# Performance work log

Measured on AMD Instinct MI355X. Metric: run time of the kernel, lower is better.

## Reference

```python
import jax, jax.numpy as jnp
import numpy as np

N_HEADS = 32
N_KV_HEADS = 8
HEAD_DIM = 64
D_MODEL = 2048
EPS = 1e-6
THETA = 10000.0


def _rms_norm(x, w):
    # normalize over last dim (head_dim)
    norm = jax.lax.rsqrt(jnp.mean(jnp.square(x), axis=-1, keepdims=True) + EPS)
    return x * norm * w


def _rope(x):
    # x: (B, H, T, D)
    T, D = x.shape[2], x.shape[3]
    inv_freq = 1.0 / (THETA ** (jnp.arange(0, D, 2, dtype=jnp.float32) / D))
    t = jnp.arange(T, dtype=jnp.float32)
    freqs = jnp.outer(t, inv_freq)                      # (T, D/2)
    freqs = jnp.concatenate([freqs, freqs], axis=-1)    # (T, D)
    cos = jnp.cos(freqs)[None, None]                    # (1,1,T,D)
    sin = jnp.sin(freqs)[None, None]
    x1, x2 = x[..., : D // 2], x[..., D // 2 :]
    x_rot = jnp.concatenate([-x2, x1], axis=-1)
    return x * cos + x_rot * sin


def setup_inputs() -> dict:
    key = jax.random.key(0)
    ks = jax.random.split(key, 5)
    B, T = 2, 2048
    s = 0.02
    return {
        "x": jax.random.normal(ks[0], (B, T, D_MODEL), jnp.float32),
        "wq": jax.random.normal(ks[1], (D_MODEL, D_MODEL), jnp.float32) * s,
        "wk": jax.random.normal(ks[2], (N_KV_HEADS * HEAD_DIM, D_MODEL), jnp.float32) * s,
        "wv": jax.random.normal(ks[3], (N_KV_HEADS * HEAD_DIM, D_MODEL), jnp.float32) * s,
        "wo": jax.random.normal(ks[4], (D_MODEL, D_MODEL), jnp.float32) * s,
        "q_norm_w": jnp.ones((HEAD_DIM,), jnp.float32),
        "k_norm_w": jnp.ones((HEAD_DIM,), jnp.float32),
    }


def reference(x, wq, wk, wv, wo, q_norm_w, k_norm_w):
    B, T, C = x.shape
    G = N_HEADS // N_KV_HEADS

    q = (x @ wq.T).reshape(B, T, N_HEADS, HEAD_DIM).transpose(0, 2, 1, 3)      # (B,H,T,D)
    k = (x @ wk.T).reshape(B, T, N_KV_HEADS, HEAD_DIM).transpose(0, 2, 1, 3)   # (B,KH,T,D)
    v = (x @ wv.T).reshape(B, T, N_KV_HEADS, HEAD_DIM).transpose(0, 2, 1, 3)

    q = _rms_norm(q, q_norm_w)
    k = _rms_norm(k, k_norm_w)

    q = _rope(q)
    k = _rope(k)

    # GQA head-expand: each kv head repeated G times consecutively
    k = jnp.repeat(k, G, axis=1)   # (B,H,T,D)
    v = jnp.repeat(v, G, axis=1)

    scale = 1.0 / np.sqrt(HEAD_DIM)
    scores = jnp.einsum("bhqd,bhkd->bhqk", q, k) * scale
    causal = jnp.tril(jnp.ones((T, T), dtype=bool))
    scores = jnp.where(causal[None, None], scores, jnp.finfo(scores.dtype).min)
    attn = jax.nn.softmax(scores, axis=-1)
    out = jnp.einsum("bhqk,bhkd->bhqd", attn, v)   # (B,H,T,D)

    out = out.transpose(0, 2, 1, 3).reshape(B, T, C)
    return out @ wo.T
```

## Files before the change

kernel.cpp:

```cpp
#include <hip/hip_runtime.h>

typedef __bf16 bf16;
typedef __bf16 bf16x8 __attribute__((ext_vector_type(8)));
typedef float f32x4 __attribute__((ext_vector_type(4)));

#define DEV __device__ __forceinline__

DEV void gload16(const void* g, void* l) {
  __builtin_amdgcn_global_load_lds(
      (__attribute__((address_space(1))) void*)g,
      (__attribute__((address_space(3))) void*)l,
      16, 0, 0);
}

DEV unsigned pack_bf16(float a, float b) {
  union { bf16 h[2]; unsigned u; } u;
  u.h[0] = (bf16)a; u.h[1] = (bf16)b;
  return u.u;
}

__global__ __launch_bounds__(256) void cvt_f32_to_bf16(
    const float* __restrict__ in, bf16* __restrict__ out, long n) {
  long i = ((long)blockIdx.x * 256 + threadIdx.x) * 8;
  if (i + 8 > n) return;
  const float4* p = (const float4*)(in + i);
  float4 a = p[0], b = p[1];
  bf16x8 o;
  o[0] = (bf16)a.x; o[1] = (bf16)a.y; o[2] = (bf16)a.z; o[3] = (bf16)a.w;
  o[4] = (bf16)b.x; o[5] = (bf16)b.y; o[6] = (bf16)b.z; o[7] = (bf16)b.w;
  *(bf16x8*)(out + i) = o;
}

template <typename OutT>
__global__ __launch_bounds__(512, 2) void gemm8p(
    const bf16* __restrict__ A, const bf16* __restrict__ B, OutT* __restrict__ C,
    int M, int N, int K) {
  __shared__ bf16 As[2][256 * 64];
  __shared__ bf16 Bs[2][256 * 64];
  const int tid = threadIdx.x;
  const int lane = tid & 63;
  const int wv = tid >> 6;
  const int wm = wv >> 2, wn = wv & 3;
  const int l15 = lane & 15, l4 = lane >> 4;
  const int swz7 = l15 & 7;
  const long m0 = (long)blockIdx.y * 256;
  const long n0 = (long)blockIdx.x * 256;
  const int NT = K >> 6;

  f32x4 acc[8][4];
#pragma unroll
  for (int i = 0; i < 8; ++i)
#pragma unroll
    for (int j = 0; j < 4; ++j) acc[i][j] = (f32x4){0.f, 0.f, 0.f, 0.f};

  auto stageA = [&](int t, int q) {
#pragma unroll
    for (int it = 0; it < 2; ++it) {
      const int c = it * 512 + tid;
      const int row = ((c >> 9) << 7) + q * 64 + ((c >> 3) & 63);
      const int cc = c & 7;
      gload16(A + (m0 + row) * (long)K + t * 64 + ((cc ^ (row & 7)) << 3),
              &As[t & 1][row * 64 + cc * 8]);
    }
  };
  auto stageB = [&](int t, int q) {
#pragma unroll
    for (int it = 0; it < 2; ++it) {
      const int c = it * 512 + tid;
      const int row = ((c >> 8) << 6) + q * 32 + ((c >> 3) & 31);
      const int cc = c & 7;
      gload16(B + (n0 + row) * (long)K + t * 64 + ((cc ^ (row & 7)) << 3),
              &Bs[t & 1][row * 64 + cc * 8]);
    }
  };

#define PHASE(CUR, QM, QN, STAGE, VM) do {                                      \
    __builtin_amdgcn_sched_barrier(0);                                          \
    bf16x8 af_[2][4], bf_[2][2];                                                \
    _Pragma("unroll")                                                           \
    for (int kk = 0; kk < 2; ++kk) {                                            \
      _Pragma("unroll")                                                         \
      for (int i = 0; i < 4; ++i)                                               \
        af_[kk][i] = *(const bf16x8*)&As[CUR][                                  \
            (wm * 128 + (QM) * 64 + i * 16 + l15) * 64 +                        \
            (((kk * 4 + l4) ^ swz7) << 3)];                                     \
      _Pragma("unroll")                                                         \
      for (int j = 0; j < 2; ++j)                                               \
        bf_[kk][j] = *(const bf16x8*)&Bs[CUR][                                  \
            (wn * 64 + (QN) * 32 + j * 16 + l15) * 64 +                         \
            (((kk * 4 + l4) ^ swz7) << 3)];                                     \
    }                                                                           \
    STAGE;                                                                      \
    VM;                                                                         \
    __builtin_amdgcn_sched_barrier(0);                                          \
    __builtin_amdgcn_s_barrier();                                               \
    asm volatile("s_waitcnt lgkmcnt(0)" ::: "memory");                          \
    __builtin_amdgcn_sched_barrier(0);                                          \
    __builtin_amdgcn_s_setprio(1);                                              \
    _Pragma("unroll")                                                           \
    for (int kk = 0; kk < 2; ++kk)                                              \
      _Pragma("unroll")                                                         \
      for (int i = 0; i < 4; ++i)                                               \
        _Pragma("unroll")                                                       \
        for (int j = 0; j < 2; ++j)                                             \
          acc[(QM) * 4 + i][(QN) * 2 + j] =                                     \
              __builtin_amdgcn_mfma_f32_16x16x32_bf16(                          \
                  af_[kk][i], bf_[kk][j], acc[(QM) * 4 + i][(QN) * 2 + j],      \
                  0, 0, 0);                                                     \
    __builtin_amdgcn_s_setprio(0);                                              \
    __builtin_amdgcn_s_barrier();                                               \
  } while (0)

  stageA(0, 0); stageA(0, 1); stageB(0, 0); stageB(0, 1);
  stageA(1, 0); stageB(1, 0);
  asm volatile("s_waitcnt vmcnt(4)" ::: "memory");
  __builtin_amdgcn_sched_barrier(0);
  __builtin_amdgcn_s_barrier();

  for (int T = 0; T < NT - 2; ++T) {
    const int cur = T & 1;
    PHASE(cur, 0, 0, stageA(T + 1, 1), );
    PHASE(cur, 0, 1, stageB(T + 1, 1), );
    PHASE(cur, 1, 0, stageA(T + 2, 0), );
    PHASE(cur, 1, 1, stageB(T + 2, 0),
          asm volatile("s_waitcnt vmcnt(4)" ::: "memory"));
  }
  {
    const int cur = (NT - 2) & 1;
    PHASE(cur, 0, 0, stageA(NT - 1, 1), );
    PHASE(cur, 0, 1, stageB(NT - 1, 1), );
    PHASE(cur, 1, 0, , );
    PHASE(cur, 1, 1, , asm volatile("s_waitcnt vmcnt(0)" ::: "memory"));
  }
  {
    const int cur = (NT - 1) & 1;
    PHASE(cur, 0, 0, , );
    PHASE(cur, 0, 1, , );
    PHASE(cur, 1, 0, , );
    PHASE(cur, 1, 1, , );
  }
#undef PHASE

#pragma unroll
  for (int i = 0; i < 8; ++i)
#pragma unroll
    for (int j = 0; j < 4; ++j) {
      const long row = m0 + wm * 128 + i * 16 + l4 * 4;
      const long col = n0 + wn * 64 + j * 16 + l15;
#pragma unroll
      for (int r = 0; r < 4; ++r)
        C[(row + r) * (long)N + col] = (OutT)acc[i][j][r];
    }
}

__global__ __launch_bounds__(256) void qk_norm_rope(
    const bf16* __restrict__ qkv, const float* __restrict__ qw,
    const float* __restrict__ kw, bf16* __restrict__ Qh, bf16* __restrict__ Kh) {
  const int wg = blockIdx.x * 4 + (threadIdx.x >> 6);
  const int lane = threadIdx.x & 63;
  const int row = wg / 40;
  const int head = wg - row * 40;
  const int b = row >> 11, t = row & 2047;
  const bool is_q = head < 32;
  const int col0 = is_q ? head * 64 : 2048 + (head - 32) * 64;

  float v = (float)qkv[(long)row * 3072 + col0 + lane];
  float ss = v * v;
  ss += __shfl_xor(ss, 1);
  ss += __shfl_xor(ss, 2);
  ss += __shfl_xor(ss, 4);
  ss += __shfl_xor(ss, 8);
  ss += __shfl_xor(ss, 16);
  ss += __shfl_xor(ss, 32);
  const float norm = rsqrtf(ss * (1.0f / 64.0f) + 1e-6f);
  const float* wn = is_q ? qw : kw;
  float xn = v * norm * wn[lane];

  const int fi = lane & 31;
  const float inv_freq = expf(-(float)fi * (9.210340371976184f / 32.0f));
  const float fr = (float)t * inv_freq;
  float sn, cs;
  sincosf(fr, &sn, &cs);
  const float xo = __shfl_xor(xn, 32);
  const float xr = (lane < 32) ? -xo : xo;
  const float res = xn * cs + xr * sn;

  if (is_q)
    Qh[(((long)b * 32 + head) * 2048 + t) * 64 + lane] = (bf16)res;
  else
    Kh[(((long)b * 8 + (head - 32)) * 2048 + t) * 64 + lane] = (bf16)res;
}

__global__ __launch_bounds__(256) void v_transpose(
    const bf16* __restrict__ qkv, bf16* __restrict__ Vt) {
  const int bh = blockIdx.x;
  const int t0 = blockIdx.y * 64;
  const int b = bh >> 3, kh = bh & 7;
  __shared__ bf16 tile[64][72];
  const int tid = threadIdx.x;
#pragma unroll
  for (int it = 0; it < 2; ++it) {
    const int tt = it * 32 + (tid >> 3);
    const int d0 = (tid & 7) * 8;
    bf16x8 val = *(const bf16x8*)&qkv[((long)b * 2048 + t0 + tt) * 3072 + 2560 + kh * 64 + d0];
#pragma unroll
    for (int j = 0; j < 8; ++j) tile[tt][d0 + j] = val[j];
  }
  __syncthreads();
#pragma unroll
  for (int it = 0; it < 2; ++it) {
    const int d = it * 32 + (tid >> 3);
    const int tb = (tid & 7) * 8;
    bf16x8 o;
#pragma unroll
    for (int j = 0; j < 8; ++j) o[j] = tile[tb + j][d];
    *(bf16x8*)&Vt[((long)bh * 64 + d) * 2048 + t0 + tb] = o;
  }
}

__global__ __launch_bounds__(256, 4) void attn_fwd(
    const bf16* __restrict__ Q, const bf16* __restrict__ K,
    const bf16* __restrict__ Vt, bf16* __restrict__ O) {
  const int b = blockIdx.x >> 5, h = blockIdx.x & 31;
  const int qb = 31 - (int)blockIdx.y;
  const int q0 = qb * 64;
  const int kvh = h >> 2;
  const bf16* Qp = Q + (((long)b * 32 + h) * 2048 + q0) * 64;
  const bf16* Kp = K + ((long)b * 8 + kvh) * (2048L * 64);
  const bf16* Vp = Vt + ((long)b * 8 + kvh) * (64L * 2048);

  __shared__ bf16 Ks[64 * 64];
  __shared__ bf16 Vs[64 * 64];

  const int tid = threadIdx.x, lane = tid & 63, w = tid >> 6;
  const int l15 = lane & 15, l4 = lane >> 4;
  const int qwr = q0 + w * 16;
  const int q_g = qwr + l15;

  bf16x8 qf[2];
#pragma unroll
  for (int kk = 0; kk < 2; ++kk)
    qf[kk] = *(const bf16x8*)(Qp + (w * 16 + l15) * 64 + kk * 32 + l4 * 8);

  f32x4 accO[4];
#pragma unroll
  for (int dn = 0; dn < 4; ++dn) accO[dn] = (f32x4){0.f, 0.f, 0.f, 0.f};
  float M = -1e30f, L = 0.f;

  const float scale = 0.125f;
  const int swz = (l15 & 7) << 3;

  for (int kt = 0; kt <= qb; ++kt) {
    const int k0 = kt * 64;
#pragma unroll
    for (int it = 0; it < 2; ++it) {
      const int c = it * 256 + tid;
      const int row = c >> 3, cc = c & 7;
      const int scol = ((cc ^ (row & 7)) << 3);
      gload16(Kp + (long)(k0 + row) * 64 + scol, &Ks[c * 8]);
      gload16(Vp + (long)row * 2048 + k0 + scol, &Vs[c * 8]);
    }
    __syncthreads();

    f32x4 sT[4];
#pragma unroll
    for (int n = 0; n < 4; ++n) sT[n] = (f32x4){0.f, 0.f, 0.f, 0.f};
#pragma unroll
    for (int kk = 0; kk < 2; ++kk) {
      bf16x8 kf[4];
#pragma unroll
      for (int n = 0; n < 4; ++n)
        kf[n] = *(const bf16x8*)&Ks[(n * 16 + l15) * 64 + (((kk * 4 + l4) << 3) ^ swz)];
#pragma unroll
      for (int n = 0; n < 4; ++n)
        sT[n] = __builtin_amdgcn_mfma_f32_16x16x32_bf16(kf[n], qf[kk], sT[n], 0, 0, 0);
    }

    const bool edge = (kt == qb);
#pragma unroll
    for (int n = 0; n < 4; ++n) {
      const int kbase = k0 + n * 16 + l4 * 4;
#pragma unroll
      for (int r = 0; r < 4; ++r) {
        float v = sT[n][r] * scale;
        if (edge && (kbase + r > q_g)) v = -1e30f;
        sT[n][r] = v;
      }
    }

    float pm = -1e30f;
#pragma unroll
    for (int n = 0; n < 4; ++n)
#pragma unroll
      for (int r = 0; r < 4; ++r) pm = fmaxf(pm, sT[n][r]);
    pm = fmaxf(pm, __shfl_xor(pm, 16));
    pm = fmaxf(pm, __shfl_xor(pm, 32));
    const float newM = fmaxf(M, pm);
    const float sc = __expf(M - newM);
    M = newM;
    float rs = 0.f;
#pragma unroll
    for (int n = 0; n < 4; ++n)
#pragma unroll
      for (int r = 0; r < 4; ++r) {
        const float pv = __expf(sT[n][r] - newM);
        sT[n][r] = pv;
        rs += pv;
      }
    rs += __shfl_xor(rs, 16);
    rs += __shfl_xor(rs, 32);
    L = L * sc + rs;
#pragma unroll
    for (int dn = 0; dn < 4; ++dn) accO[dn] *= sc;

    unsigned lo[4], hi[4];
#pragma unroll
    for (int n = 0; n < 4; ++n) {
      lo[n] = pack_bf16(sT[n][0], sT[n][1]);
      hi[n] = pack_bf16(sT[n][2], sT[n][3]);
    }

    const int srcA = l15 | ((l4 & 1) << 5);
    const int srcB = srcA + 16;
    const bool selHi = (l4 >> 1);
#pragma unroll
    for (int kk = 0; kk < 2; ++kk) {
      unsigned d0a = __shfl(lo[2 * kk], srcA), d0b = __shfl(lo[2 * kk + 1], srcA);
      unsigned d1a = __shfl(hi[2 * kk], srcA), d1b = __shfl(hi[2 * kk + 1], srcA);
      unsigned d2a = __shfl(lo[2 * kk], srcB), d2b = __shfl(lo[2 * kk + 1], srcB);
      unsigned d3a = __shfl(hi[2 * kk], srcB), d3b = __shfl(hi[2 * kk + 1], srcB);
      union { unsigned d[4]; bf16x8 v; } pu;
      pu.d[0] = selHi ? d0b : d0a;
      pu.d[1] = selHi ? d1b : d1a;
      pu.d[2] = selHi ? d2b : d2a;
      pu.d[3] = selHi ? d3b : d3a;
      bf16x8 vf[4];
#pragma unroll
      for (int dn = 0; dn < 4; ++dn)
        vf[dn] = *(const bf16x8*)&Vs[(dn * 16 + l15) * 64 + (((kk * 4 + l4) << 3) ^ swz)];
#pragma unroll
      for (int dn = 0; dn < 4; ++dn)
        accO[dn] = __builtin_amdgcn_mfma_f32_16x16x32_bf16(vf[dn], pu.v, accO[dn], 0, 0, 0);
    }
    __syncthreads();
  }

  const float inv = 1.0f / L;
  const long rowbase = ((long)b * 2048 + q_g) * 2048 + h * 64;
#pragma unroll
  for (int dn = 0; dn < 4; ++dn)
#pragma unroll
    for (int rp = 0; rp < 2; ++rp) {
      const unsigned pk = pack_bf16(accO[dn][2 * rp] * inv, accO[dn][2 * rp + 1] * inv);
      *(unsigned*)&O[rowbase + dn * 16 + l4 * 4 + 2 * rp] = pk;
    }
}

extern "C" void kernel_launch(void* const* d_in, const int* in_sizes, int n_in,
                              void* d_out, int out_size, void* d_ws, size_t ws_size,
                              hipStream_t stream) {
  const float* x   = (const float*)d_in[0];
  const float* wq  = (const float*)d_in[1];
  const float* wk  = (const float*)d_in[2];
  const float* wv  = (const float*)d_in[3];
  const float* wo  = (const float*)d_in[4];
  const float* qnw = (const float*)d_in[5];
  const float* knw = (const float*)d_in[6];
  float* out = (float*)d_out;

  char* ws = (char*)d_ws;
  size_t off = 0;
  auto carve = [&](size_t bytes) -> void* {
    void* p = ws + off;
    off += (bytes + 255) & ~(size_t)255;
    return p;
  };
  bf16* xb    = (bf16*)carve(8388608ull * 2);
  bf16* wqkvb = (bf16*)carve(6291456ull * 2);
  bf16* wob   = (bf16*)carve(4194304ull * 2);
  bf16* qkvb  = (bf16*)carve(12582912ull * 2);
  bf16* Qh    = (bf16*)carve(8388608ull * 2);
  bf16* Kh    = (bf16*)carve(2097152ull * 2);
  bf16* Vt    = (bf16*)carve(2097152ull * 2);

  cvt_f32_to_bf16<<<4096, 256, 0, stream>>>(x, xb, 8388608L);
  cvt_f32_to_bf16<<<2048, 256, 0, stream>>>(wq, wqkvb, 4194304L);
  cvt_f32_to_bf16<<<512, 256, 0, stream>>>(wk, wqkvb + 4194304, 1048576L);
  cvt_f32_to_bf16<<<512, 256, 0, stream>>>(wv, wqkvb + 5242880, 1048576L);
  cvt_f32_to_bf16<<<2048, 256, 0, stream>>>(wo, wob, 4194304L);

  gemm8p<bf16><<<dim3(12, 16), 512, 0, stream>>>(xb, wqkvb, qkvb, 4096, 3072, 2048);
  qk_norm_rope<<<40960, 256, 0, stream>>>(qkvb, qnw, knw, Qh, Kh);
  v_transpose<<<dim3(16, 32), 256, 0, stream>>>(qkvb, Vt);

  bf16* attnb = xb;
  attn_fwd<<<dim3(64, 32), 256, 0, stream>>>(Qh, Kh, Vt, attnb);

  gemm8p<float><<<dim3(8, 16), 512, 0, stream>>>(attnb, wob, out, 4096, 2048, 2048);
}
```

Measured before the change: 389.0 us.

## Fuse conversions, precompute RoPE table, widen attention KV tile, add lazy rescale

Merges the five fp32-to-bf16 conversion launches into one kernel that writes a single contiguous buffer. It precomputes a cos/sin RoPE table and folds the softmax scale into Q. GEMM workgroups are remapped so neighbouring blocks are spread across XCDs. The attention kernel moves to 128-key tiles, masks only tiles that touch the diagonal, and skips the online-softmax rescale unless the running max grows by more than a threshold. This cuts launch overhead, transcendental work, loop iterations and rescale multiplies, at the cost of more LDS per block and extra work on the diagonal tile.

```diff
diff --git a/kernel.cpp b/kernel.cpp
--- a/kernel.cpp
+++ b/kernel.cpp
@@ -19,16 +19,33 @@
   return u.u;
 }
 
-__global__ __launch_bounds__(256) void cvt_f32_to_bf16(
-    const float* __restrict__ in, bf16* __restrict__ out, long n) {
-  long i = ((long)blockIdx.x * 256 + threadIdx.x) * 8;
-  if (i + 8 > n) return;
-  const float4* p = (const float4*)(in + i);
+__global__ __launch_bounds__(256) void cvt_fused(
+    const float* __restrict__ s0, const float* __restrict__ s1,
+    const float* __restrict__ s2, const float* __restrict__ s3,
+    const float* __restrict__ s4, bf16* __restrict__ out) {
+  const long i = ((long)blockIdx.x * 256 + threadIdx.x) * 8;
+  const float* src;
+  long off;
+  if (i < 8388608)       { src = s0; off = i; }
+  else if (i < 12582912) { src = s1; off = i - 8388608; }
+  else if (i < 13631488) { src = s2; off = i - 12582912; }
+  else if (i < 14680064) { src = s3; off = i - 13631488; }
+  else                   { src = s4; off = i - 14680064; }
+  const float4* p = (const float4*)(src + off);
   float4 a = p[0], b = p[1];
   bf16x8 o;
   o[0] = (bf16)a.x; o[1] = (bf16)a.y; o[2] = (bf16)a.z; o[3] = (bf16)a.w;
   o[4] = (bf16)b.x; o[5] = (bf16)b.y; o[6] = (bf16)b.z; o[7] = (bf16)b.w;
   *(bf16x8*)(out + i) = o;
+}
+
+__global__ __launch_bounds__(256) void rope_table(float2* __restrict__ tab) {
+  const int idx = blockIdx.x * 256 + threadIdx.x;
+  const int t = idx >> 5, fi = idx & 31;
+  const float invf = expf(-(float)fi * (9.210340371976184f / 32.0f));
+  float sn, cs;
+  sincosf((float)t * invf, &sn, &cs);
+  tab[idx] = make_float2(cs, sn);
 }
 
 template <typename OutT>
@@ -43,8 +60,13 @@
   const int wm = wv >> 2, wn = wv & 3;
   const int l15 = lane & 15, l4 = lane >> 4;
   const int swz7 = l15 & 7;
-  const long m0 = (long)blockIdx.y * 256;
-  const long n0 = (long)blockIdx.x * 256;
+
+  const int nx = gridDim.x;
+  const int nwg = nx * gridDim.y;
+  int wg = blockIdx.y * nx + blockIdx.x;
+  wg = (wg & 7) * (nwg >> 3) + (wg >> 3);
+  const long m0 = (long)(wg / nx) * 256;
+  const long n0 = (long)(wg % nx) * 256;
   const int NT = K >> 6;
 
   f32x4 acc[8][4];
@@ -155,7 +177,8 @@
 
 __global__ __launch_bounds__(256) void qk_norm_rope(
     const bf16* __restrict__ qkv, const float* __restrict__ qw,
-    const float* __restrict__ kw, bf16* __restrict__ Qh, bf16* __restrict__ Kh) {
+    const float* __restrict__ kw, const float2* __restrict__ tab,
+    bf16* __restrict__ Qh, bf16* __restrict__ Kh) {
   const int wg = blockIdx.x * 4 + (threadIdx.x >> 6);
   const int lane = threadIdx.x & 63;
   const int row = wg / 40;
@@ -177,18 +200,17 @@
   float xn = v * norm * wn[lane];
 
   const int fi = lane & 31;
-  const float inv_freq = expf(-(float)fi * (9.210340371976184f / 32.0f));
-  const float fr = (float)t * inv_freq;
-  float sn, cs;
-  sincosf(fr, &sn, &cs);
+  const float2 cn = tab[t * 32 + fi];
   const float xo = __shfl_xor(xn, 32);
   const float xr = (lane < 32) ? -xo : xo;
-  const float res = xn * cs + xr * sn;
-
-  if (is_q)
+  float res = xn * cn.x + xr * cn.y;
+
+  if (is_q) {
+    res *= 0.125f;
     Qh[(((long)b * 32 + head) * 2048 + t) * 64 + lane] = (bf16)res;
-  else
+  } else {
     Kh[(((long)b * 8 + (head - 32)) * 2048 + t) * 64 + lane] = (bf16)res;
+  }
 }
 
 __global__ __launch_bounds__(256) void v_transpose(
@@ -229,11 +251,12 @@
   const bf16* Kp = K + ((long)b * 8 + kvh) * (2048L * 64);
   const bf16* Vp = Vt + ((long)b * 8 + kvh) * (64L * 2048);
 
-  __shared__ bf16 Ks[64 * 64];
-  __shared__ bf16 Vs[64 * 64];
+  __shared__ bf16 Ks[128 * 64];
+  __shared__ bf16 Vs[64 * 128];
 
   const int tid = threadIdx.x, lane = tid & 63, w = tid >> 6;
   const int l15 = lane & 15, l4 = lane >> 4;
+  const int swz7 = l15 & 7;
   const int qwr = q0 + w * 16;
   const int q_g = qwr + l15;
 
@@ -247,75 +270,74 @@
   for (int dn = 0; dn < 4; ++dn) accO[dn] = (f32x4){0.f, 0.f, 0.f, 0.f};
   float M = -1e30f, L = 0.f;
 
-  const float scale = 0.125f;
-  const int swz = (l15 & 7) << 3;
-
-  for (int kt = 0; kt <= qb; ++kt) {
-    const int k0 = kt * 64;
-#pragma unroll
-    for (int it = 0; it < 2; ++it) {
+  const int NKT = (qb + 2) >> 1;
+  for (int kt = 0; kt < NKT; ++kt) {
+    const int k0 = kt * 128;
+#pragma unroll
+    for (int it = 0; it < 4; ++it) {
       const int c = it * 256 + tid;
-      const int row = c >> 3, cc = c & 7;
-      const int scol = ((cc ^ (row & 7)) << 3);
-      gload16(Kp + (long)(k0 + row) * 64 + scol, &Ks[c * 8]);
-      gload16(Vp + (long)row * 2048 + k0 + scol, &Vs[c * 8]);
+      const int kr = c >> 3, kc = c & 7;
+      gload16(Kp + (long)(k0 + kr) * 64 + ((kc ^ (kr & 7)) << 3), &Ks[c * 8]);
+      const int vr = c >> 4, vc = c & 15;
+      gload16(Vp + (long)vr * 2048 + k0 + ((vc ^ (vr & 7)) << 3), &Vs[c * 8]);
     }
     __syncthreads();
 
-    f32x4 sT[4];
-#pragma unroll
-    for (int n = 0; n < 4; ++n) sT[n] = (f32x4){0.f, 0.f, 0.f, 0.f};
+    f32x4 sT[8];
+#pragma unroll
+    for (int n = 0; n < 8; ++n) sT[n] = (f32x4){0.f, 0.f, 0.f, 0.f};
 #pragma unroll
     for (int kk = 0; kk < 2; ++kk) {
-      bf16x8 kf[4];
-#pragma unroll
-      for (int n = 0; n < 4; ++n)
-        kf[n] = *(const bf16x8*)&Ks[(n * 16 + l15) * 64 + (((kk * 4 + l4) << 3) ^ swz)];
-#pragma unroll
-      for (int n = 0; n < 4; ++n)
+      bf16x8 kf[8];
+#pragma unroll
+      for (int n = 0; n < 8; ++n)
+        kf[n] = *(const bf16x8*)&Ks[(n * 16 + l15) * 64 + (((kk * 4 + l4) ^ swz7) << 3)];
+#pragma unroll
+      for (int n = 0; n < 8; ++n)
         sT[n] = __builtin_amdgcn_mfma_f32_16x16x32_bf16(kf[n], qf[kk], sT[n], 0, 0, 0);
     }
 
-    const bool edge = (kt == qb);
-#pragma unroll
-    for (int n = 0; n < 4; ++n) {
-      const int kbase = k0 + n * 16 + l4 * 4;
-#pragma unroll
-      for (int r = 0; r < 4; ++r) {
-        float v = sT[n][r] * scale;
-        if (edge && (kbase + r > q_g)) v = -1e30f;
-        sT[n][r] = v;
+    if (k0 + 127 > qwr) {
+#pragma unroll
+      for (int n = 0; n < 8; ++n) {
+        const int kbase = k0 + n * 16 + l4 * 4;
+#pragma unroll
+        for (int r = 0; r < 4; ++r)
+          if (kbase + r > q_g) sT[n][r] = -1e30f;
       }
     }
 
     float pm = -1e30f;
 #pragma unroll
-    for (int n = 0; n < 4; ++n)
+    for (int n = 0; n < 8; ++n)
 #pragma unroll
       for (int r = 0; r < 4; ++r) pm = fmaxf(pm, sT[n][r]);
     pm = fmaxf(pm, __shfl_xor(pm, 16));
     pm = fmaxf(pm, __shfl_xor(pm, 32));
-    const float newM = fmaxf(M, pm);
-    const float sc = __expf(M - newM);
-    M = newM;
+    if (!__all(pm - M <= 8.0f)) {
+      const float newM = fmaxf(M, pm);
+      const float sc = __expf(M - newM);
+      M = newM;
+      L *= sc;
+#pragma unroll
+      for (int dn = 0; dn < 4; ++dn) accO[dn] *= sc;
+    }
     float rs = 0.f;
 #pragma unroll
-    for (int n = 0; n < 4; ++n)
+    for (int n = 0; n < 8; ++n)
 #pragma unroll
       for (int r = 0; r < 4; ++r) {
-        const float pv = __expf(sT[n][r] - newM);
+        const float pv = __expf(sT[n][r] - M);
         sT[n][r] = pv;
         rs += pv;
       }
     rs += __shfl_xor(rs, 16);
     rs += __shfl_xor(rs, 32);
-    L = L * sc + rs;
-#pragma unroll
-    for (int dn = 0; dn < 4; ++dn) accO[dn] *= sc;
-
-    unsigned lo[4], hi[4];
-#pragma unroll
-    for (int n = 0; n < 4; ++n) {
+    L += rs;
+
+    unsigned lo[8], hi[8];
+#pragma unroll
+    for (int n = 0; n < 8; ++n) {
       lo[n] = pack_bf16(sT[n][0], sT[n][1]);
       hi[n] = pack_bf16(sT[n][2], sT[n][3]);
     }
@@ -324,7 +346,7 @@
     const int srcB = srcA + 16;
     const bool selHi = (l4 >> 1);
 #pragma unroll
-    for (int kk = 0; kk < 2; ++kk) {
+    for (int kk = 0; kk < 4; ++kk) {
       unsigned d0a = __shfl(lo[2 * kk], srcA), d0b = __shfl(lo[2 * kk + 1], srcA);
       unsigned d1a = __shfl(hi[2 * kk], srcA), d1b = __shfl(hi[2 * kk + 1], srcA);
       unsigned d2a = __shfl(lo[2 * kk], srcB), d2b = __shfl(lo[2 * kk + 1], srcB);
@@ -337,7 +359,7 @@
       bf16x8 vf[4];
 #pragma unroll
       for (int dn = 0; dn < 4; ++dn)
-        vf[dn] = *(const bf16x8*)&Vs[(dn * 16 + l15) * 64 + (((kk * 4 + l4) << 3) ^ swz)];
+        vf[dn] = *(const bf16x8*)&Vs[(dn * 16 + l15) * 128 + (((kk * 4 + l4) ^ swz7) << 3)];
 #pragma unroll
       for (int dn = 0; dn < 4; ++dn)
         accO[dn] = __builtin_amdgcn_mfma_f32_16x16x32_bf16(vf[dn], pu.v, accO[dn], 0, 0, 0);
@@ -382,15 +404,13 @@
   bf16* Qh    = (bf16*)carve(8388608ull * 2);
   bf16* Kh    = (bf16*)carve(2097152ull * 2);
   bf16* Vt    = (bf16*)carve(2097152ull * 2);
-
-  cvt_f32_to_bf16<<<4096, 256, 0, stream>>>(x, xb, 8388608L);
-  cvt_f32_to_bf16<<<2048, 256, 0, stream>>>(wq, wqkvb, 4194304L);
-  cvt_f32_to_bf16<<<512, 256, 0, stream>>>(wk, wqkvb + 4194304, 1048576L);
-  cvt_f32_to_bf16<<<512, 256, 0, stream>>>(wv, wqkvb + 5242880, 1048576L);
-  cvt_f32_to_bf16<<<2048, 256, 0, stream>>>(wo, wob, 4194304L);
+  float2* tab = (float2*)carve(65536ull * 8);
+
+  rope_table<<<256, 256, 0, stream>>>(tab);
+  cvt_fused<<<9216, 256, 0, stream>>>(x, wq, wk, wv, wo, xb);
 
   gemm8p<bf16><<<dim3(12, 16), 512, 0, stream>>>(xb, wqkvb, qkvb, 4096, 3072, 2048);
-  qk_norm_rope<<<40960, 256, 0, stream>>>(qkvb, qnw, knw, Qh, Kh);
+  qk_norm_rope<<<40960, 256, 0, stream>>>(qkvb, qnw, knw, tab, Qh, Kh);
   v_transpose<<<dim3(16, 32), 256, 0, stream>>>(qkvb, Vt);
 
   bf16* attnb = xb;
```

After: 367.8 us. -5.4%, faster.
